# Kernel tuning notes

Hardware: AMD Instinct MI355X
Metric: run time of the kernel (lower is better)

The kernel has to match this reference:

```python
import jax, jax.numpy as jnp
import numpy as np

D_MODEL = 1024
N_HEADS = 16
D_HEAD = D_MODEL // N_HEADS


def setup_inputs() -> dict:
    key = jax.random.key(0)
    ks = jax.random.split(key, 9)
    s = 1.0 / np.sqrt(D_MODEL)
    def lin(kw, kb):
        W = jax.random.uniform(kw, (D_MODEL, D_MODEL), jnp.float32, -s, s)
        b = jax.random.uniform(kb, (D_MODEL,), jnp.float32, -s, s)
        return W, b
    Wq, bq = lin(ks[0], ks[1])
    Wk, bk = lin(ks[2], ks[3])
    Wv, bv = lin(ks[4], ks[5])
    Wo, bo = lin(ks[6], ks[7])
    x = jax.random.normal(ks[8], (4, 2048, D_MODEL), jnp.float32)
    return {"x": x, "Wq": Wq, "bq": bq, "Wk": Wk, "bk": bk,
            "Wv": Wv, "bv": bv, "Wo": Wo, "bo": bo}


def reference(x, Wq, bq, Wk, bk, Wv, bv, Wo, bo):
    B, T, C = x.shape
    # torch Linear: y = x @ W.T + b
    Q = x @ Wq.T + bq
    K = x @ Wk.T + bk
    V = x @ Wv.T + bv
    # [B, H, T, Dh]
    Q = Q.reshape(B, T, N_HEADS, D_HEAD).transpose(0, 2, 1, 3)
    K = K.reshape(B, T, N_HEADS, D_HEAD).transpose(0, 2, 1, 3)
    V = V.reshape(B, T, N_HEADS, D_HEAD).transpose(0, 2, 1, 3)
    scale = jnp.float32(np.sqrt(D_HEAD))
    scores = jnp.einsum('bhqd,bhkd->bhqk', Q, K) / scale
    causal = jnp.tril(jnp.ones((T, T), dtype=bool))  # True where allowed
    scores = jnp.where(causal, scores, jnp.float32(-jnp.inf))
    attn = jax.nn.softmax(scores, axis=-1)
    out = jnp.einsum('bhqk,bhkd->bhqd', attn, V)
    out = out.transpose(0, 2, 1, 3).reshape(B, T, C)
    return out @ Wo.T + bo
```

## Files before the change

### kernel.cpp

```cpp
#include <hip/hip_runtime.h>
#include <hip/hip_bf16.h>


typedef float f32x4 __attribute__((ext_vector_type(4)));
typedef __bf16 bf16x8 __attribute__((ext_vector_type(8)));

#define DEVI __device__ __forceinline__

#define QSCALE 0.1803368801111204f

template<int N> struct IC { static constexpr int value = N; };

DEVI ushort f2b(float x) {
  __hip_bfloat16 h = __float2bfloat16(x);
  return __builtin_bit_cast(ushort, h);
}

DEVI unsigned int pkbf(float a, float b) {
#if __has_builtin(__builtin_amdgcn_cvt_pk_bf16_f32)
  typedef __bf16 bf16x2 __attribute__((ext_vector_type(2)));
  bf16x2 r = __builtin_amdgcn_cvt_pk_bf16_f32(a, b);
  return __builtin_bit_cast(unsigned int, r);
#else
  return (unsigned int)f2b(a) | ((unsigned int)f2b(b) << 16);
#endif
}

DEVI bf16x8 ldsFrag(const ushort* p) {
  return __builtin_bit_cast(bf16x8, *(const uint4*)p);
}

DEVI f32x4 mfma16(bf16x8 a, bf16x8 b, f32x4 c) {
  return __builtin_amdgcn_mfma_f32_16x16x32_bf16(a, b, c, 0, 0, 0);
}

DEVI void gload_lds16(const ushort* g, ushort* l) {
  __builtin_amdgcn_global_load_lds(
      (const __attribute__((address_space(1))) unsigned int*)g,
      (__attribute__((address_space(3))) unsigned int*)l, 16, 0, 0);
}

#define SBAR() do { __builtin_amdgcn_sched_barrier(0); \
                    __builtin_amdgcn_s_barrier();      \
                    __builtin_amdgcn_sched_barrier(0); } while (0)

__global__ void k_cvtAll(const float4* __restrict__ x,
                         const float4* __restrict__ w0, const float4* __restrict__ w1,
                         const float4* __restrict__ w2, const float4* __restrict__ w3,
                         ushort4* __restrict__ xb, ushort4* __restrict__ wcat) {
  const int blk = blockIdx.x;
  const int i = blk * 256 + threadIdx.x;
  float4 f;
  ushort4* dst;
  int di;
  if (blk < 8192) {
    f = x[i]; dst = xb; di = i;
  } else {
    const int wi = i - 8192 * 256;
    const int sel = wi >> 18;
    const float4* src = (sel == 0) ? w0 : (sel == 1) ? w1 : (sel == 2) ? w2 : w3;
    f = src[wi & 262143]; dst = wcat; di = wi;
  }
  ushort4 o;
  o.x = f2b(f.x); o.y = f2b(f.y); o.z = f2b(f.z); o.w = f2b(f.w);
  dst[di] = o;
}

__global__ __launch_bounds__(512, 2)
void k_gemmQKV(const ushort* __restrict__ A, const ushort* __restrict__ W,
               const float* __restrict__ bq, const float* __restrict__ bk,
               const float* __restrict__ bv,
               ushort* __restrict__ oQ, ushort* __restrict__ oK,
               ushort* __restrict__ oV) {
  __shared__ ushort As[2][256 * 64];
  __shared__ ushort Bs[2][384 * 64];
  const int tid = threadIdx.x;
  const int wave = tid >> 6, lane = tid & 63;
  const int col = lane & 15, quad = lane >> 4;
  const int id = blockIdx.x;
  const int xcd = id & 7, idx = id >> 3;
  const int m0 = (xcd * 4 + (idx & 3)) * 256;
  const int nb = idx >> 2;
  const int wm = (wave >> 2) * 128;
  const int wn = (wave & 3) * 64;
  const int wnv = (wave & 3) * 32;
  const bool matQ = (nb < 4);

  const int grow = lane >> 3;
  const int gchunk = ((lane & 7) ^ grow) * 8;
  const int cswz = col & 7;
  const ushort* Ag = A + (size_t)(m0 + wave * 32 + grow) * 1024 + gchunk;

  auto bptr = [&](int u) {
    const int br = wave * 48 + u * 8;
    const int wr = (br < 256) ? (nb * 256 + br + grow)
                              : (2048 + nb * 128 + (br - 256) + grow);
    return W + (size_t)wr * 1024 + gchunk;
  };

  f32x4 aq[8][4] = {};
  f32x4 av[8][2] = {};
  bf16x8 bfr[4], bfv[2];

  auto stage6 = [&](int t1) {
    const int buf = t1 & 1;
    const int ks = t1 * 64;
#pragma unroll
    for (int u = 0; u < 4; ++u)
      gload_lds16(Ag + (size_t)u * 8 * 1024 + ks, &As[buf][(wave * 32 + u * 8) * 64]);
#pragma unroll
    for (int u = 0; u < 2; ++u)
      gload_lds16(bptr(u) + ks, &Bs[buf][(wave * 48 + u * 8) * 64]);
  };
  auto stage4 = [&](int t1) {
    const int buf = t1 & 1;
    const int ks = t1 * 64;
#pragma unroll
    for (int u = 2; u < 6; ++u)
      gload_lds16(bptr(u) + ks, &Bs[buf][(wave * 48 + u * 8) * 64]);
  };

  auto phase = [&](int p, int h, int kk, bool rdB, int dr, auto stg) {
    const int ko = ((kk * 4 + quad) ^ cswz) * 8;
    bf16x8 af[4];
#pragma unroll
    for (int i = 0; i < 4; ++i)
      af[i] = ldsFrag(&As[p][(wm + h * 64 + i * 16 + col) * 64 + ko]);
    if (rdB) {
#pragma unroll
      for (int j = 0; j < 4; ++j)
        bfr[j] = ldsFrag(&Bs[p][(wn + j * 16 + col) * 64 + ko]);
#pragma unroll
      for (int j = 0; j < 2; ++j)
        bfv[j] = ldsFrag(&Bs[p][(256 + wnv + j * 16 + col) * 64 + ko]);
    }
    stg();
    SBAR();
    asm volatile("s_waitcnt lgkmcnt(0)" ::: "memory");
    __builtin_amdgcn_sched_barrier(0);
    __builtin_amdgcn_s_setprio(1);
#pragma unroll
    for (int i = 0; i < 4; ++i)
#pragma unroll
      for (int j = 0; j < 4; ++j)
        aq[h * 4 + i][j] = mfma16(bfr[j], af[i], aq[h * 4 + i][j]);
#pragma unroll
    for (int i = 0; i < 4; ++i)
#pragma unroll
      for (int j = 0; j < 2; ++j)
        av[h * 4 + i][j] = mfma16(af[i], bfv[j], av[h * 4 + i][j]);
    __builtin_amdgcn_s_setprio(0);
    if (dr) { asm volatile("s_waitcnt vmcnt(0)" ::: "memory"); }
    SBAR();
  };

  stage6(0); stage4(0);
  asm volatile("s_waitcnt vmcnt(0)" ::: "memory");
  SBAR();

  for (int t = 0; t < 16; ++t) {
    const int p = t & 1;
    const bool st = (t < 15);
    phase(p, 0, 0, true,  0,  [&] { if (st) stage6(t + 1); });
    phase(p, 1, 0, false, 0,  [&] { if (st) stage4(t + 1); });
    phase(p, 0, 1, true,  0,  [&] {});
    phase(p, 1, 1, false, st ? 1 : 0, [&] {});
  }

  {
    ushort* dst = matQ ? oQ : oK;
    const float* bias = matQ ? bq : bk;
    const float sc = matQ ? QSCALE : 1.0f;
#pragma unroll
    for (int h = 0; h < 2; ++h)
#pragma unroll
      for (int j = 0; j < 4; ++j) {
        const int nl = (nb & 3) * 256 + wn + j * 16 + quad * 4;
        const int hh = nl >> 6, dh0 = nl & 63;
        const float4 bb = *(const float4*)&bias[nl];
#pragma unroll
        for (int i = 0; i < 4; ++i) {
          const int m = m0 + wm + h * 64 + i * 16 + col;
          const int b = m >> 11, t = m & 2047;
          ushort4 pk;
          pk.x = f2b((aq[h * 4 + i][j][0] + bb.x) * sc);
          pk.y = f2b((aq[h * 4 + i][j][1] + bb.y) * sc);
          pk.z = f2b((aq[h * 4 + i][j][2] + bb.z) * sc);
          pk.w = f2b((aq[h * 4 + i][j][3] + bb.w) * sc);
          *(ushort4*)&dst[(((size_t)(b * 16 + hh) * 2048) + t) * 64 + dh0] = pk;
        }
      }
  }
  {
#pragma unroll
    for (int h = 0; h < 2; ++h)
#pragma unroll
      for (int j = 0; j < 2; ++j) {
        const int nl = nb * 128 + wnv + j * 16 + col;
        const int hh = nl >> 6, dh = nl & 63;
        const float bn = bv[nl];
#pragma unroll
        for (int i = 0; i < 4; ++i) {
          const int mBase = m0 + wm + h * 64 + i * 16 + quad * 4;
          const int b = mBase >> 11, t = mBase & 2047;
          ushort4 pk;
          pk.x = f2b(av[h * 4 + i][j][0] + bn);
          pk.y = f2b(av[h * 4 + i][j][1] + bn);
          pk.z = f2b(av[h * 4 + i][j][2] + bn);
          pk.w = f2b(av[h * 4 + i][j][3] + bn);
          *(ushort4*)&oV[(((size_t)(b * 16 + hh) * 64) + dh) * 2048 + t] = pk;
        }
      }
  }
}

__global__ __launch_bounds__(512, 2)
void k_gemmP(const ushort* __restrict__ A, const ushort* __restrict__ W,
             const float* __restrict__ b0, float* __restrict__ outF) {
  __shared__ ushort As[3 * 128 * 64];
  __shared__ ushort Bs[3 * 256 * 64];
  const int tid = threadIdx.x;
  const int wave = tid >> 6, lane = tid & 63;
  const int col = lane & 15, quad = lane >> 4;
  const int id = blockIdx.x;
  const int s_ = id >> 3;
  const int m0 = ((id & 7) * 8 + (s_ & 7)) * 128;
  const int n0 = (s_ >> 3) * 256;
  const int wm = (wave >> 2) * 64, wn = (wave & 3) * 64;
  f32x4 acc[4][4] = {};

  const int grow = lane >> 3;
  const int gchunk = ((lane & 7) ^ grow) * 8;
  const int cswz = col & 7;
  const ushort* Ag = A + (size_t)(m0 + wave * 16 + grow) * 1024 + gchunk;
  const ushort* Wg = W + (size_t)(n0 + wave * 32 + grow) * 1024 + gchunk;
  ushort* AsW = &As[wave * 1024];
  ushort* BsW = &Bs[wave * 2048];

  auto stageA = [&](int ks, int sb) {
    gload_lds16(Ag + ks,        AsW + sb * 8192);
    gload_lds16(Ag + ks + 8192, AsW + sb * 8192 + 512);
  };
  auto stageBh = [&](int ks, int sb, int h) {
    const ushort* sp = Wg + ks + h * 16384;
    ushort* dp = BsW + sb * 16384 + h * 1024;
    gload_lds16(sp,        dp);
    gload_lds16(sp + 8192, dp + 512);
  };

  auto phase = [&](int cur, int kk, auto stagef) {
    const int ko = ((kk * 4 + quad) ^ cswz) * 8;
    const ushort* Ab = &As[cur * 8192];
    const ushort* Bb = &Bs[cur * 16384];
    bf16x8 af[4], bfr[4];
#pragma unroll
    for (int i = 0; i < 4; ++i)
      af[i] = ldsFrag(&Ab[(wm + i * 16 + col) * 64 + ko]);
#pragma unroll
    for (int j = 0; j < 4; ++j)
      bfr[j] = ldsFrag(&Bb[(wn + j * 16 + col) * 64 + ko]);
    stagef();
    SBAR();
    __builtin_amdgcn_s_setprio(1);
#pragma unroll
    for (int i = 0; i < 4; ++i)
#pragma unroll
      for (int j = 0; j < 4; ++j)
        acc[i][j] = mfma16(bfr[j], af[i], acc[i][j]);
    __builtin_amdgcn_s_setprio(0);
  };

  stageA(0, 0);  stageBh(0, 0, 0);  stageBh(0, 0, 1);
  stageA(64, 1); stageBh(64, 1, 0); stageBh(64, 1, 1);
  asm volatile("s_waitcnt vmcnt(6)" ::: "memory");
  SBAR();

  int r0 = 0, r1 = 1, r2 = 2;
  for (int t = 0; t < 14; ++t) {
    const int ks = (t + 2) * 64;
    phase(r0, 0, [&] { stageA(ks, r2); stageBh(ks, r2, 0); });
    SBAR();
    phase(r0, 1, [&] { stageBh(ks, r2, 1); });
    asm volatile("s_waitcnt vmcnt(6)" ::: "memory");
    SBAR();
    const int tmp = r0; r0 = r1; r1 = r2; r2 = tmp;
  }
  phase(r0, 0, [&] {});
  SBAR();
  phase(r0, 1, [&] {});
  asm volatile("s_waitcnt vmcnt(0)" ::: "memory");
  SBAR();
  phase(r1, 0, [&] {});
  SBAR();
  phase(r1, 1, [&] {});

#pragma unroll
  for (int j = 0; j < 4; ++j) {
    const int nb = n0 + wn + j * 16 + quad * 4;
    const float4 bb = *(const float4*)&b0[nb];
#pragma unroll
    for (int i = 0; i < 4; ++i) {
      const int m = m0 + wm + i * 16 + col;
      float4 v;
      v.x = acc[i][j][0] + bb.x;
      v.y = acc[i][j][1] + bb.y;
      v.z = acc[i][j][2] + bb.z;
      v.w = acc[i][j][3] + bb.w;
      *(float4*)&outF[(size_t)m * 1024 + nb] = v;
    }
  }
}

__global__ __launch_bounds__(512, 4)
void k_attn(const ushort* __restrict__ Q, const ushort* __restrict__ K,
            const ushort* __restrict__ Vt, ushort* __restrict__ AO) {
  __shared__ ushort Ks[2 * 4096];
  __shared__ ushort Vs[2 * 4096];
  __shared__ ushort Os[512];
  __shared__ ushort Ps[16 * 16 * 72];
  const int tid = threadIdx.x;
  const int wave = tid >> 6, lane = tid & 63;
  const int col = lane & 15, quad = lane >> 4;
  const int id = blockIdx.x;
  const int bh = (id & 7) * 8 + ((id >> 3) & 7);
  const int g = id >> 6;
  const int t = (id < 256) ? (7 - g) : (g - 4);
  const int q0 = t * 256;
  const ushort* Qg = Q + (size_t)bh * 2048 * 64;
  const ushort* Kg = K + (size_t)bh * 2048 * 64;
  const ushort* Vg = Vt + (size_t)bh * 64 * 2048;

  if (tid < 128) {
    const ushort one = 0x3F80;
    ushort4 zv;
    if (tid < 8) { zv.x = one; zv.y = one; zv.z = one; zv.w = one; }
    else         { zv.x = 0;   zv.y = 0;   zv.z = 0;   zv.w = 0;   }
    *(ushort4*)&Os[tid * 4] = zv;
  }

  const int grow = lane >> 3;
  const int gchunk = ((lane & 7) ^ grow) * 8;
  const int cswz = col & 7;
  ushort* Pw0 = &Ps[((wave * 2 + 0) * 16 + col) * 72];
  ushort* Pw1 = &Ps[((wave * 2 + 1) * 16 + col) * 72];

  bf16x8 qf[2][2];
#pragma unroll
  for (int s = 0; s < 2; ++s) {
    const ushort* p = Qg + (q0 + wave * 32 + s * 16 + col) * 64 + quad * 8;
    qf[s][0] = __builtin_bit_cast(bf16x8, *(const uint4*)p);
    qf[s][1] = __builtin_bit_cast(bf16x8, *(const uint4*)(p + 32));
  }

  f32x4 o[2][4] = {};
  f32x4 la[2] = {};

  const ushort* kPtr = Kg + (wave * 8 + grow) * 64 + gchunk;
  const ushort* vPtr = Vg + (size_t)(wave * 8 + grow) * 2048 + gchunk;

  auto stage = [&](auto bufc) {
    constexpr int BUF = decltype(bufc)::value;
    gload_lds16(kPtr, &Ks[BUF * 4096 + wave * 512]);
    gload_lds16(vPtr, &Vs[BUF * 4096 + wave * 512]);
    kPtr += 64 * 64;
    vPtr += 64;
  };

  auto step = [&](auto bufc, auto maskc, int j0) {
    constexpr int BUF = decltype(bufc)::value;
    constexpr bool MASKED = (decltype(maskc)::value != 0);
    const ushort* Kb = &Ks[BUF * 4096];
    const ushort* Vb = &Vs[BUF * 4096];
    bf16x8 kf[4][2];
#pragma unroll
    for (int i = 0; i < 4; ++i) {
      kf[i][0] = ldsFrag(&Kb[(i * 16 + col) * 64 + (((0 * 4 + quad) ^ cswz) * 8)]);
      kf[i][1] = ldsFrag(&Kb[(i * 16 + col) * 64 + (((1 * 4 + quad) ^ cswz) * 8)]);
    }
#pragma unroll
    for (int s = 0; s < 2; ++s) {
      ushort* Pw = s ? Pw1 : Pw0;
      const int dlim = MASKED ? (q0 + wave * 32 + s * 16 + col - j0 - quad * 4) : 0;
#pragma unroll
      for (int i = 0; i < 4; ++i) {
        f32x4 z = {0.f, 0.f, 0.f, 0.f};
        f32x4 sv = mfma16(kf[i][0], qf[s][0], z);
        sv = mfma16(kf[i][1], qf[s][1], sv);
        if (MASKED) {
#pragma unroll
          for (int r = 0; r < 4; ++r)
            if (i * 16 + r > dlim) sv[r] = -1e30f;
        }
        f32x4 pv;
#pragma unroll
        for (int r = 0; r < 4; ++r) pv[r] = __builtin_amdgcn_exp2f(sv[r]);
        uint2 pk;
        pk.x = pkbf(pv[0], pv[1]);
        pk.y = pkbf(pv[2], pv[3]);
        *(uint2*)&Pw[i * 16 + quad * 4] = pk;
      }
    }
    bf16x8 osf = ldsFrag(&Os[col * 32 + quad * 8]);
#pragma unroll
    for (int c = 0; c < 2; ++c) {
      bf16x8 pb0 = ldsFrag(&Pw0[c * 32 + quad * 8]);
      bf16x8 pb1 = ldsFrag(&Pw1[c * 32 + quad * 8]);
      la[0] = mfma16(osf, pb0, la[0]);
      la[1] = mfma16(osf, pb1, la[1]);
#pragma unroll
      for (int i = 0; i < 4; ++i) {
        bf16x8 vf = ldsFrag(&Vb[(i * 16 + col) * 64 + (((c * 4 + quad) ^ cswz) * 8)]);
        o[0][i] = mfma16(vf, pb0, o[0][i]);
        o[1][i] = mfma16(vf, pb1, o[1][i]);
      }
    }
  };

  __syncthreads();
  stage(IC<0>{});
  for (int it2 = 0; it2 < 2 * t; ++it2) {
    __syncthreads();
    stage(IC<1>{});
    step(IC<0>{}, IC<0>{}, 0);
    __syncthreads();
    stage(IC<0>{});
    step(IC<1>{}, IC<0>{}, 0);
  }
  __syncthreads();
  stage(IC<1>{});
  step(IC<0>{}, IC<1>{}, q0);
  __syncthreads();
  stage(IC<0>{});
  if (wave >= 2) step(IC<1>{}, IC<1>{}, q0 + 64);
  __syncthreads();
  stage(IC<1>{});
  if (wave >= 4) step(IC<0>{}, IC<1>{}, q0 + 128);
  __syncthreads();
  if (wave >= 6) step(IC<1>{}, IC<1>{}, q0 + 192);

  const float invs[2] = {1.0f / __shfl(la[0][0], col), 1.0f / __shfl(la[1][0], col)};
  const int b = bh >> 4, h = bh & 15;
#pragma unroll
  for (int s = 0; s < 2; ++s) {
    const float inv = invs[s];
    const int tq = q0 + wave * 32 + s * 16 + col;
    ushort* dst = AO + (size_t)(b * 2048 + tq) * 1024 + h * 64;
#pragma unroll
    for (int i = 0; i < 4; ++i) {
      f32x4 v = o[s][i];
      ushort4 pk;
      pk.x = f2b(v[0] * inv);
      pk.y = f2b(v[1] * inv);
      pk.z = f2b(v[2] * inv);
      pk.w = f2b(v[3] * inv);
      *(ushort4*)&dst[i * 16 + quad * 4] = pk;
    }
  }
}

extern "C" void kernel_launch(void* const* d_in, const int* in_sizes, int n_in,
                              void* d_out, int out_size, void* d_ws, size_t ws_size,
                              hipStream_t stream) {
  const float* x  = (const float*)d_in[0];
  const float* Wq = (const float*)d_in[1];
  const float* bq = (const float*)d_in[2];
  const float* Wk = (const float*)d_in[3];
  const float* bk = (const float*)d_in[4];
  const float* Wv = (const float*)d_in[5];
  const float* bv = (const float*)d_in[6];
  const float* Wo = (const float*)d_in[7];
  const float* bo = (const float*)d_in[8];
  float* out = (float*)d_out;

  char* ws = (char*)d_ws;
  ushort* xb    = (ushort*)ws;
  ushort* Wcat  = (ushort*)(ws + (size_t)16 * 1024 * 1024);
  ushort* Wob   = Wcat + (size_t)3 * 1024 * 1024;
  ushort* Qh    = (ushort*)(ws + (size_t)24 * 1024 * 1024);
  ushort* Kh    = Qh + (size_t)8192 * 1024;
  ushort* Vt    = Kh + (size_t)8192 * 1024;
  ushort* AO    = Vt + (size_t)8192 * 1024;

  k_cvtAll<<<12288, 256, 0, stream>>>((const float4*)x,
                                      (const float4*)Wq, (const float4*)Wk,
                                      (const float4*)Wv, (const float4*)Wo,
                                      (ushort4*)xb, (ushort4*)Wcat);

  k_gemmQKV<<<256, 512, 0, stream>>>(xb, Wcat, bq, bk, bv, Qh, Kh, Vt);

  k_attn<<<512, 512, 0, stream>>>(Qh, Kh, Vt, AO);

  k_gemmP<<<256, 512, 0, stream>>>(AO, Wob, bo, out);
}
```

Measured before the change: 245.9 us.

## Fuse convert, QKV GEMM, attention and projection into one cooperative persistent kernel

Replaces the four separate launches (convert, QKV GEMM, attention, output GEMM) with a single cooperative kernel of 256 blocks that runs the stages in sequence, separated by grid-wide syncs. Shared memory is one union buffer reused by each stage. Attention now handles two query tiles per block, pairing tile t with 7-t to balance the causal work. The aim is to remove launch gaps and tail effects between kernels. The cost is grid.sync overhead, lower occupancy in attention (previously 512 blocks at 4 per CU, now 256 blocks with large static LDS), and a convert stage limited to 256 blocks.

```diff
diff --git a/kernel.cpp b/kernel.cpp
--- a/kernel.cpp
+++ b/kernel.cpp
@@ -1,5 +1,8 @@
 #include <hip/hip_runtime.h>
 #include <hip/hip_bf16.h>
+#include <hip/hip_cooperative_groups.h>
+
+namespace cg = cooperative_groups;
 
 
 typedef float f32x4 __attribute__((ext_vector_type(4)));
@@ -44,416 +47,431 @@
                     __builtin_amdgcn_s_barrier();      \
                     __builtin_amdgcn_sched_barrier(0); } while (0)
 
-__global__ void k_cvtAll(const float4* __restrict__ x,
-                         const float4* __restrict__ w0, const float4* __restrict__ w1,
-                         const float4* __restrict__ w2, const float4* __restrict__ w3,
-                         ushort4* __restrict__ xb, ushort4* __restrict__ wcat) {
-  const int blk = blockIdx.x;
-  const int i = blk * 256 + threadIdx.x;
-  float4 f;
-  ushort4* dst;
-  int di;
-  if (blk < 8192) {
-    f = x[i]; dst = xb; di = i;
-  } else {
-    const int wi = i - 8192 * 256;
-    const int sel = wi >> 18;
-    const float4* src = (sel == 0) ? w0 : (sel == 1) ? w1 : (sel == 2) ? w2 : w3;
-    f = src[wi & 262143]; dst = wcat; di = wi;
-  }
-  ushort4 o;
-  o.x = f2b(f.x); o.y = f2b(f.y); o.z = f2b(f.z); o.w = f2b(f.w);
-  dst[di] = o;
-}
-
 __global__ __launch_bounds__(512, 2)
-void k_gemmQKV(const ushort* __restrict__ A, const ushort* __restrict__ W,
-               const float* __restrict__ bq, const float* __restrict__ bk,
-               const float* __restrict__ bv,
-               ushort* __restrict__ oQ, ushort* __restrict__ oK,
-               ushort* __restrict__ oV) {
-  __shared__ ushort As[2][256 * 64];
-  __shared__ ushort Bs[2][384 * 64];
+void k_fused(const float4* __restrict__ x4,
+             const float4* __restrict__ w0, const float4* __restrict__ w1,
+             const float4* __restrict__ w2, const float4* __restrict__ w3,
+             const float* __restrict__ bq, const float* __restrict__ bk,
+             const float* __restrict__ bv, const float* __restrict__ bo,
+             float* __restrict__ outF,
+             ushort* __restrict__ xb, ushort* __restrict__ Wcat,
+             ushort* __restrict__ Wob,
+             ushort* __restrict__ Qh, ushort* __restrict__ Kh,
+             ushort* __restrict__ Vt, ushort* __restrict__ AO) {
+  __shared__ __align__(16) char smem[163840];
+  cg::grid_group grid = cg::this_grid();
+
   const int tid = threadIdx.x;
   const int wave = tid >> 6, lane = tid & 63;
   const int col = lane & 15, quad = lane >> 4;
   const int id = blockIdx.x;
-  const int xcd = id & 7, idx = id >> 3;
-  const int m0 = (xcd * 4 + (idx & 3)) * 256;
-  const int nb = idx >> 2;
-  const int wm = (wave >> 2) * 128;
-  const int wn = (wave & 3) * 64;
-  const int wnv = (wave & 3) * 32;
-  const bool matQ = (nb < 4);
-
-  const int grow = lane >> 3;
-  const int gchunk = ((lane & 7) ^ grow) * 8;
-  const int cswz = col & 7;
-  const ushort* Ag = A + (size_t)(m0 + wave * 32 + grow) * 1024 + gchunk;
-
-  auto bptr = [&](int u) {
-    const int br = wave * 48 + u * 8;
-    const int wr = (br < 256) ? (nb * 256 + br + grow)
-                              : (2048 + nb * 128 + (br - 256) + grow);
-    return W + (size_t)wr * 1024 + gchunk;
-  };
-
-  f32x4 aq[8][4] = {};
-  f32x4 av[8][2] = {};
-  bf16x8 bfr[4], bfv[2];
-
-  auto stage6 = [&](int t1) {
-    const int buf = t1 & 1;
-    const int ks = t1 * 64;
-#pragma unroll
-    for (int u = 0; u < 4; ++u)
-      gload_lds16(Ag + (size_t)u * 8 * 1024 + ks, &As[buf][(wave * 32 + u * 8) * 64]);
-#pragma unroll
-    for (int u = 0; u < 2; ++u)
-      gload_lds16(bptr(u) + ks, &Bs[buf][(wave * 48 + u * 8) * 64]);
-  };
-  auto stage4 = [&](int t1) {
-    const int buf = t1 & 1;
-    const int ks = t1 * 64;
-#pragma unroll
-    for (int u = 2; u < 6; ++u)
-      gload_lds16(bptr(u) + ks, &Bs[buf][(wave * 48 + u * 8) * 64]);
-  };
-
-  auto phase = [&](int p, int h, int kk, bool rdB, int dr, auto stg) {
-    const int ko = ((kk * 4 + quad) ^ cswz) * 8;
-    bf16x8 af[4];
-#pragma unroll
-    for (int i = 0; i < 4; ++i)
-      af[i] = ldsFrag(&As[p][(wm + h * 64 + i * 16 + col) * 64 + ko]);
-    if (rdB) {
-#pragma unroll
-      for (int j = 0; j < 4; ++j)
-        bfr[j] = ldsFrag(&Bs[p][(wn + j * 16 + col) * 64 + ko]);
-#pragma unroll
-      for (int j = 0; j < 2; ++j)
-        bfv[j] = ldsFrag(&Bs[p][(256 + wnv + j * 16 + col) * 64 + ko]);
-    }
-    stg();
+
+  {
+    ushort4* xb4 = (ushort4*)xb;
+    ushort4* wc4 = (ushort4*)Wcat;
+    const int stride = 256 * 512;
+    for (int idx = id * 512 + tid; idx < 3145728; idx += stride) {
+      float4 f;
+      ushort4* dst;
+      int di;
+      if (idx < 2097152) {
+        f = x4[idx]; dst = xb4; di = idx;
+      } else {
+        const int wi = idx - 2097152;
+        const int sel = wi >> 18;
+        const float4* src = (sel == 0) ? w0 : (sel == 1) ? w1 : (sel == 2) ? w2 : w3;
+        f = src[wi & 262143]; dst = wc4; di = wi;
+      }
+      ushort4 o;
+      o.x = f2b(f.x); o.y = f2b(f.y); o.z = f2b(f.z); o.w = f2b(f.w);
+      dst[di] = o;
+    }
+  }
+
+  grid.sync();
+
+  {
+    ushort* As = (ushort*)smem;
+    ushort* Bs = (ushort*)(smem + 65536);
+    const ushort* A = xb;
+    const ushort* W = Wcat;
+    const int xcd = id & 7, idx = id >> 3;
+    const int m0 = (xcd * 4 + (idx & 3)) * 256;
+    const int nb = idx >> 2;
+    const int wm = (wave >> 2) * 128;
+    const int wn = (wave & 3) * 64;
+    const int wnv = (wave & 3) * 32;
+    const bool matQ = (nb < 4);
+
+    const int grow = lane >> 3;
+    const int gchunk = ((lane & 7) ^ grow) * 8;
+    const int cswz = col & 7;
+    const ushort* Ag = A + (size_t)(m0 + wave * 32 + grow) * 1024 + gchunk;
+
+    auto bptr = [&](int u) {
+      const int br = wave * 48 + u * 8;
+      const int wr = (br < 256) ? (nb * 256 + br + grow)
+                                : (2048 + nb * 128 + (br - 256) + grow);
+      return W + (size_t)wr * 1024 + gchunk;
+    };
+
+    f32x4 aq[8][4] = {};
+    f32x4 av[8][2] = {};
+    bf16x8 bfr[4], bfv[2];
+
+    auto stage6 = [&](int t1) {
+      const int buf = t1 & 1;
+      const int ks = t1 * 64;
+#pragma unroll
+      for (int u = 0; u < 4; ++u)
+        gload_lds16(Ag + (size_t)u * 8 * 1024 + ks,
+                    &As[buf * 16384 + (wave * 32 + u * 8) * 64]);
+#pragma unroll
+      for (int u = 0; u < 2; ++u)
+        gload_lds16(bptr(u) + ks, &Bs[buf * 24576 + (wave * 48 + u * 8) * 64]);
+    };
+    auto stage4 = [&](int t1) {
+      const int buf = t1 & 1;
+      const int ks = t1 * 64;
+#pragma unroll
+      for (int u = 2; u < 6; ++u)
+        gload_lds16(bptr(u) + ks, &Bs[buf * 24576 + (wave * 48 + u * 8) * 64]);
+    };
+
+    auto phase = [&](int p, int h, int kk, bool rdB, int dr, auto stg) {
+      const int ko = ((kk * 4 + quad) ^ cswz) * 8;
+      bf16x8 af[4];
+#pragma unroll
+      for (int i = 0; i < 4; ++i)
+        af[i] = ldsFrag(&As[p * 16384 + (wm + h * 64 + i * 16 + col) * 64 + ko]);
+      if (rdB) {
+#pragma unroll
+        for (int j = 0; j < 4; ++j)
+          bfr[j] = ldsFrag(&Bs[p * 24576 + (wn + j * 16 + col) * 64 + ko]);
+#pragma unroll
+        for (int j = 0; j < 2; ++j)
+          bfv[j] = ldsFrag(&Bs[p * 24576 + (256 + wnv + j * 16 + col) * 64 + ko]);
+      }
+      stg();
+      SBAR();
+      asm volatile("s_waitcnt lgkmcnt(0)" ::: "memory");
+      __builtin_amdgcn_sched_barrier(0);
+      __builtin_amdgcn_s_setprio(1);
+#pragma unroll
+      for (int i = 0; i < 4; ++i)
+#pragma unroll
+        for (int j = 0; j < 4; ++j)
+          aq[h * 4 + i][j] = mfma16(bfr[j], af[i], aq[h * 4 + i][j]);
+#pragma unroll
+      for (int i = 0; i < 4; ++i)
+#pragma unroll
+        for (int j = 0; j < 2; ++j)
+          av[h * 4 + i][j] = mfma16(af[i], bfv[j], av[h * 4 + i][j]);
+      __builtin_amdgcn_s_setprio(0);
+      if (dr) { asm volatile("s_waitcnt vmcnt(0)" ::: "memory"); }
+      SBAR();
+    };
+
+    stage6(0); stage4(0);
+    asm volatile("s_waitcnt vmcnt(0)" ::: "memory");
     SBAR();
-    asm volatile("s_waitcnt lgkmcnt(0)" ::: "memory");
-    __builtin_amdgcn_sched_barrier(0);
-    __builtin_amdgcn_s_setprio(1);
-#pragma unroll
-    for (int i = 0; i < 4; ++i)
-#pragma unroll
-      for (int j = 0; j < 4; ++j)
-        aq[h * 4 + i][j] = mfma16(bfr[j], af[i], aq[h * 4 + i][j]);
-#pragma unroll
-    for (int i = 0; i < 4; ++i)
-#pragma unroll
-      for (int j = 0; j < 2; ++j)
-        av[h * 4 + i][j] = mfma16(af[i], bfv[j], av[h * 4 + i][j]);
-    __builtin_amdgcn_s_setprio(0);
-    if (dr) { asm volatile("s_waitcnt vmcnt(0)" ::: "memory"); }
-    SBAR();
-  };
-
-  stage6(0); stage4(0);
-  asm volatile("s_waitcnt vmcnt(0)" ::: "memory");
-  SBAR();
-
-  for (int t = 0; t < 16; ++t) {
-    const int p = t & 1;
-    const bool st = (t < 15);
-    phase(p, 0, 0, true,  0,  [&] { if (st) stage6(t + 1); });
-    phase(p, 1, 0, false, 0,  [&] { if (st) stage4(t + 1); });
-    phase(p, 0, 1, true,  0,  [&] {});
-    phase(p, 1, 1, false, st ? 1 : 0, [&] {});
+
+    for (int t = 0; t < 16; ++t) {
+      const int p = t & 1;
+      const bool st = (t < 15);
+      phase(p, 0, 0, true,  0,  [&] { if (st) stage6(t + 1); });
+      phase(p, 1, 0, false, 0,  [&] { if (st) stage4(t + 1); });
+      phase(p, 0, 1, true,  0,  [&] {});
+      phase(p, 1, 1, false, st ? 1 : 0, [&] {});
+    }
+
+    {
+      ushort* dst = matQ ? Qh : Kh;
+      const float* bias = matQ ? bq : bk;
+      const float sc = matQ ? QSCALE : 1.0f;
+#pragma unroll
+      for (int h = 0; h < 2; ++h)
+#pragma unroll
+        for (int j = 0; j < 4; ++j) {
+          const int nl = (nb & 3) * 256 + wn + j * 16 + quad * 4;
+          const int hh = nl >> 6, dh0 = nl & 63;
+          const float4 bb = *(const float4*)&bias[nl];
+#pragma unroll
+          for (int i = 0; i < 4; ++i) {
+            const int m = m0 + wm + h * 64 + i * 16 + col;
+            const int b = m >> 11, t = m & 2047;
+            ushort4 pk;
+            pk.x = f2b((aq[h * 4 + i][j][0] + bb.x) * sc);
+            pk.y = f2b((aq[h * 4 + i][j][1] + bb.y) * sc);
+            pk.z = f2b((aq[h * 4 + i][j][2] + bb.z) * sc);
+            pk.w = f2b((aq[h * 4 + i][j][3] + bb.w) * sc);
+            *(ushort4*)&dst[(((size_t)(b * 16 + hh) * 2048) + t) * 64 + dh0] = pk;
+          }
+        }
+    }
+    {
+#pragma unroll
+      for (int h = 0; h < 2; ++h)
+#pragma unroll
+        for (int j = 0; j < 2; ++j) {
+          const int nl = nb * 128 + wnv + j * 16 + col;
+          const int hh = nl >> 6, dh = nl & 63;
+          const float bn = bv[nl];
+#pragma unroll
+          for (int i = 0; i < 4; ++i) {
+            const int mBase = m0 + wm + h * 64 + i * 16 + quad * 4;
+            const int b = mBase >> 11, t = mBase & 2047;
+            ushort4 pk;
+            pk.x = f2b(av[h * 4 + i][j][0] + bn);
+            pk.y = f2b(av[h * 4 + i][j][1] + bn);
+            pk.z = f2b(av[h * 4 + i][j][2] + bn);
+            pk.w = f2b(av[h * 4 + i][j][3] + bn);
+            *(ushort4*)&Vt[(((size_t)(b * 16 + hh) * 64) + dh) * 2048 + t] = pk;
+          }
+        }
+    }
   }
 
+  grid.sync();
+
   {
-    ushort* dst = matQ ? oQ : oK;
-    const float* bias = matQ ? bq : bk;
-    const float sc = matQ ? QSCALE : 1.0f;
-#pragma unroll
-    for (int h = 0; h < 2; ++h)
-#pragma unroll
-      for (int j = 0; j < 4; ++j) {
-        const int nl = (nb & 3) * 256 + wn + j * 16 + quad * 4;
-        const int hh = nl >> 6, dh0 = nl & 63;
-        const float4 bb = *(const float4*)&bias[nl];
+    ushort* Ks = (ushort*)smem;
+    ushort* Vs = Ks + 8192;
+    ushort* Os = Vs + 8192;
+    ushort* Ps = Os + 512;
+    const int bh = (id & 7) * 8 + ((id >> 3) & 7);
+    const int pr = id >> 6;
+    const ushort* Qg = Qh + (size_t)bh * 2048 * 64;
+    const ushort* Kg = Kh + (size_t)bh * 2048 * 64;
+    const ushort* Vg = Vt + (size_t)bh * 64 * 2048;
+
+    __syncthreads();
+    if (tid < 128) {
+      const ushort one = 0x3F80;
+      ushort4 zv;
+      if (tid < 8) { zv.x = one; zv.y = one; zv.z = one; zv.w = one; }
+      else         { zv.x = 0;   zv.y = 0;   zv.z = 0;   zv.w = 0;   }
+      *(ushort4*)&Os[tid * 4] = zv;
+    }
+
+    const int grow = lane >> 3;
+    const int gchunk = ((lane & 7) ^ grow) * 8;
+    const int cswz = col & 7;
+    ushort* Pw0 = &Ps[((wave * 2 + 0) * 16 + col) * 72];
+    ushort* Pw1 = &Ps[((wave * 2 + 1) * 16 + col) * 72];
+
+    for (int pp = 0; pp < 2; ++pp) {
+      const int t = pp ? (7 - pr) : pr;
+      const int q0 = t * 256;
+
+      bf16x8 qf[2][2];
+#pragma unroll
+      for (int s = 0; s < 2; ++s) {
+        const ushort* p = Qg + (q0 + wave * 32 + s * 16 + col) * 64 + quad * 8;
+        qf[s][0] = __builtin_bit_cast(bf16x8, *(const uint4*)p);
+        qf[s][1] = __builtin_bit_cast(bf16x8, *(const uint4*)(p + 32));
+      }
+
+      f32x4 o[2][4] = {};
+      f32x4 la[2] = {};
+
+      const ushort* kPtr = Kg + (wave * 8 + grow) * 64 + gchunk;
+      const ushort* vPtr = Vg + (size_t)(wave * 8 + grow) * 2048 + gchunk;
+
+      auto stage = [&](auto bufc) {
+        constexpr int BUF = decltype(bufc)::value;
+        gload_lds16(kPtr, &Ks[BUF * 4096 + wave * 512]);
+        gload_lds16(vPtr, &Vs[BUF * 4096 + wave * 512]);
+        kPtr += 64 * 64;
+        vPtr += 64;
+      };
+
+      auto step = [&](auto bufc, auto maskc, int j0) {
+        constexpr int BUF = decltype(bufc)::value;
+        constexpr bool MASKED = (decltype(maskc)::value != 0);
+        const ushort* Kb = &Ks[BUF * 4096];
+        const ushort* Vb = &Vs[BUF * 4096];
+        bf16x8 kf[4][2];
 #pragma unroll
         for (int i = 0; i < 4; ++i) {
-          const int m = m0 + wm + h * 64 + i * 16 + col;
-          const int b = m >> 11, t = m & 2047;
+          kf[i][0] = ldsFrag(&Kb[(i * 16 + col) * 64 + (((0 * 4 + quad) ^ cswz) * 8)]);
+          kf[i][1] = ldsFrag(&Kb[(i * 16 + col) * 64 + (((1 * 4 + quad) ^ cswz) * 8)]);
+        }
+#pragma unroll
+        for (int s = 0; s < 2; ++s) {
+          ushort* Pw = s ? Pw1 : Pw0;
+          const int dlim = MASKED ? (q0 + wave * 32 + s * 16 + col - j0 - quad * 4) : 0;
+#pragma unroll
+          for (int i = 0; i < 4; ++i) {
+            f32x4 z = {0.f, 0.f, 0.f, 0.f};
+            f32x4 sv = mfma16(kf[i][0], qf[s][0], z);
+            sv = mfma16(kf[i][1], qf[s][1], sv);
+            if (MASKED) {
+#pragma unroll
+              for (int r = 0; r < 4; ++r)
+                if (i * 16 + r > dlim) sv[r] = -1e30f;
+            }
+            f32x4 pv;
+#pragma unroll
+            for (int r = 0; r < 4; ++r) pv[r] = __builtin_amdgcn_exp2f(sv[r]);
+            uint2 pk;
+            pk.x = pkbf(pv[0], pv[1]);
+            pk.y = pkbf(pv[2], pv[3]);
+            *(uint2*)&Pw[i * 16 + quad * 4] = pk;
+          }
+        }
+        bf16x8 osf = ldsFrag(&Os[col * 32 + quad * 8]);
+#pragma unroll
+        for (int c = 0; c < 2; ++c) {
+          bf16x8 pb0 = ldsFrag(&Pw0[c * 32 + quad * 8]);
+          bf16x8 pb1 = ldsFrag(&Pw1[c * 32 + quad * 8]);
+          la[0] = mfma16(osf, pb0, la[0]);
+          la[1] = mfma16(osf, pb1, la[1]);
+#pragma unroll
+          for (int i = 0; i < 4; ++i) {
+            bf16x8 vf = ldsFrag(&Vb[(i * 16 + col) * 64 + (((c * 4 + quad) ^ cswz) * 8)]);
+            o[0][i] = mfma16(vf, pb0, o[0][i]);
+            o[1][i] = mfma16(vf, pb1, o[1][i]);
+          }
+        }
+      };
+
+      __syncthreads();
+      stage(IC<0>{});
+      for (int it2 = 0; it2 < 2 * t; ++it2) {
+        __syncthreads();
+        stage(IC<1>{});
+        step(IC<0>{}, IC<0>{}, 0);
+        __syncthreads();
+        stage(IC<0>{});
+        step(IC<1>{}, IC<0>{}, 0);
+      }
+      __syncthreads();
+      stage(IC<1>{});
+      step(IC<0>{}, IC<1>{}, q0);
+      __syncthreads();
+      stage(IC<0>{});
+      if (wave >= 2) step(IC<1>{}, IC<1>{}, q0 + 64);
+      __syncthreads();
+      stage(IC<1>{});
+      if (wave >= 4) step(IC<0>{}, IC<1>{}, q0 + 128);
+      __syncthreads();
+      if (wave >= 6) step(IC<1>{}, IC<1>{}, q0 + 192);
+
+      const float invs[2] = {1.0f / __shfl(la[0][0], col), 1.0f / __shfl(la[1][0], col)};
+      const int b = bh >> 4, h = bh & 15;
+#pragma unroll
+      for (int s = 0; s < 2; ++s) {
+        const float inv = invs[s];
+        const int tq = q0 + wave * 32 + s * 16 + col;
+        ushort* dst = AO + (size_t)(b * 2048 + tq) * 1024 + h * 64;
+#pragma unroll
+        for (int i = 0; i < 4; ++i) {
+          f32x4 v = o[s][i];
           ushort4 pk;
-          pk.x = f2b((aq[h * 4 + i][j][0] + bb.x) * sc);
-          pk.y = f2b((aq[h * 4 + i][j][1] + bb.y) * sc);
-          pk.z = f2b((aq[h * 4 + i][j][2] + bb.z) * sc);
-          pk.w = f2b((aq[h * 4 + i][j][3] + bb.w) * sc);
-          *(ushort4*)&dst[(((size_t)(b * 16 + hh) * 2048) + t) * 64 + dh0] = pk;
+          pk.x = f2b(v[0] * inv);
+          pk.y = f2b(v[1] * inv);
+          pk.z = f2b(v[2] * inv);
+          pk.w = f2b(v[3] * inv);
+          *(ushort4*)&dst[i * 16 + quad * 4] = pk;
         }
       }
+    }
   }
+
+  grid.sync();
+
   {
-#pragma unroll
-    for (int h = 0; h < 2; ++h)
-#pragma unroll
-      for (int j = 0; j < 2; ++j) {
-        const int nl = nb * 128 + wnv + j * 16 + col;
-        const int hh = nl >> 6, dh = nl & 63;
-        const float bn = bv[nl];
-#pragma unroll
-        for (int i = 0; i < 4; ++i) {
-          const int mBase = m0 + wm + h * 64 + i * 16 + quad * 4;
-          const int b = mBase >> 11, t = mBase & 2047;
-          ushort4 pk;
-          pk.x = f2b(av[h * 4 + i][j][0] + bn);
-          pk.y = f2b(av[h * 4 + i][j][1] + bn);
-          pk.z = f2b(av[h * 4 + i][j][2] + bn);
-          pk.w = f2b(av[h * 4 + i][j][3] + bn);
-          *(ushort4*)&oV[(((size_t)(b * 16 + hh) * 64) + dh) * 2048 + t] = pk;
-        }
-      }
-  }
-}
-
-__global__ __launch_bounds__(512, 2)
-void k_gemmP(const ushort* __restrict__ A, const ushort* __restrict__ W,
-             const float* __restrict__ b0, float* __restrict__ outF) {
-  __shared__ ushort As[3 * 128 * 64];
-  __shared__ ushort Bs[3 * 256 * 64];
-  const int tid = threadIdx.x;
-  const int wave = tid >> 6, lane = tid & 63;
-  const int col = lane & 15, quad = lane >> 4;
-  const int id = blockIdx.x;
-  const int s_ = id >> 3;
-  const int m0 = ((id & 7) * 8 + (s_ & 7)) * 128;
-  const int n0 = (s_ >> 3) * 256;
-  const int wm = (wave >> 2) * 64, wn = (wave & 3) * 64;
-  f32x4 acc[4][4] = {};
-
-  const int grow = lane >> 3;
-  const int gchunk = ((lane & 7) ^ grow) * 8;
-  const int cswz = col & 7;
-  const ushort* Ag = A + (size_t)(m0 + wave * 16 + grow) * 1024 + gchunk;
-  const ushort* Wg = W + (size_t)(n0 + wave * 32 + grow) * 1024 + gchunk;
-  ushort* AsW = &As[wave * 1024];
-  ushort* BsW = &Bs[wave * 2048];
-
-  auto stageA = [&](int ks, int sb) {
-    gload_lds16(Ag + ks,        AsW + sb * 8192);
-    gload_lds16(Ag + ks + 8192, AsW + sb * 8192 + 512);
-  };
-  auto stageBh = [&](int ks, int sb, int h) {
-    const ushort* sp = Wg + ks + h * 16384;
-    ushort* dp = BsW + sb * 16384 + h * 1024;
-    gload_lds16(sp,        dp);
-    gload_lds16(sp + 8192, dp + 512);
-  };
-
-  auto phase = [&](int cur, int kk, auto stagef) {
-    const int ko = ((kk * 4 + quad) ^ cswz) * 8;
-    const ushort* Ab = &As[cur * 8192];
-    const ushort* Bb = &Bs[cur * 16384];
-    bf16x8 af[4], bfr[4];
-#pragma unroll
-    for (int i = 0; i < 4; ++i)
-      af[i] = ldsFrag(&Ab[(wm + i * 16 + col) * 64 + ko]);
-#pragma unroll
-    for (int j = 0; j < 4; ++j)
-      bfr[j] = ldsFrag(&Bb[(wn + j * 16 + col) * 64 + ko]);
-    stagef();
-    SBAR();
-    __builtin_amdgcn_s_setprio(1);
-#pragma unroll
-    for (int i = 0; i < 4; ++i)
+    ushort* As = (ushort*)smem;
+    ushort* Bs = (ushort*)(smem + 49152);
+    const ushort* A = AO;
+    const ushort* W = Wob;
+    const int s_ = id >> 3;
+    const int m0 = ((id & 7) * 8 + (s_ & 7)) * 128;
+    const int n0 = (s_ >> 3) * 256;
+    const int wm = (wave >> 2) * 64, wn = (wave & 3) * 64;
+    f32x4 acc[4][4] = {};
+
+    const int grow = lane >> 3;
+    const int gchunk = ((lane & 7) ^ grow) * 8;
+    const int cswz = col & 7;
+    const ushort* Ag = A + (size_t)(m0 + wave * 16 + grow) * 1024 + gchunk;
+    const ushort* Wg = W + (size_t)(n0 + wave * 32 + grow) * 1024 + gchunk;
+    ushort* AsW = &As[wave * 1024];
+    ushort* BsW = &Bs[wave * 2048];
+
+    auto stageA = [&](int ks, int sb) {
+      gload_lds16(Ag + ks,        AsW + sb * 8192);
+      gload_lds16(Ag + ks + 8192, AsW + sb * 8192 + 512);
+    };
+    auto stageBh = [&](int ks, int sb, int h) {
+      const ushort* sp = Wg + ks + h * 16384;
+      ushort* dp = BsW + sb * 16384 + h * 1024;
+      gload_lds16(sp,        dp);
+      gload_lds16(sp + 8192, dp + 512);
+    };
+
+    auto phase = [&](int cur, int kk, auto stagef) {
+      const int ko = ((kk * 4 + quad) ^ cswz) * 8;
+      const ushort* Ab = &As[cur * 8192];
+      const ushort* Bb = &Bs[cur * 16384];
+      bf16x8 af[4], bfr[4];
+#pragma unroll
+      for (int i = 0; i < 4; ++i)
+        af[i] = ldsFrag(&Ab[(wm + i * 16 + col) * 64 + ko]);
 #pragma unroll
       for (int j = 0; j < 4; ++j)
-        acc[i][j] = mfma16(bfr[j], af[i], acc[i][j]);
-    __builtin_amdgcn_s_setprio(0);
-  };
-
-  stageA(0, 0);  stageBh(0, 0, 0);  stageBh(0, 0, 1);
-  stageA(64, 1); stageBh(64, 1, 0); stageBh(64, 1, 1);
-  asm volatile("s_waitcnt vmcnt(6)" ::: "memory");
-  SBAR();
-
-  int r0 = 0, r1 = 1, r2 = 2;
-  for (int t = 0; t < 14; ++t) {
-    const int ks = (t + 2) * 64;
-    phase(r0, 0, [&] { stageA(ks, r2); stageBh(ks, r2, 0); });
-    SBAR();
-    phase(r0, 1, [&] { stageBh(ks, r2, 1); });
+        bfr[j] = ldsFrag(&Bb[(wn + j * 16 + col) * 64 + ko]);
+      stagef();
+      SBAR();
+      __builtin_amdgcn_s_setprio(1);
+#pragma unroll
+      for (int i = 0; i < 4; ++i)
+#pragma unroll
+        for (int j = 0; j < 4; ++j)
+          acc[i][j] = mfma16(bfr[j], af[i], acc[i][j]);
+      __builtin_amdgcn_s_setprio(0);
+    };
+
+    __syncthreads();
+    stageA(0, 0);  stageBh(0, 0, 0);  stageBh(0, 0, 1);
+    stageA(64, 1); stageBh(64, 1, 0); stageBh(64, 1, 1);
     asm volatile("s_waitcnt vmcnt(6)" ::: "memory");
     SBAR();
-    const int tmp = r0; r0 = r1; r1 = r2; r2 = tmp;
-  }
-  phase(r0, 0, [&] {});
-  SBAR();
-  phase(r0, 1, [&] {});
-  asm volatile("s_waitcnt vmcnt(0)" ::: "memory");
-  SBAR();
-  phase(r1, 0, [&] {});
-  SBAR();
-  phase(r1, 1, [&] {});
-
-#pragma unroll
-  for (int j = 0; j < 4; ++j) {
-    const int nb = n0 + wn + j * 16 + quad * 4;
-    const float4 bb = *(const float4*)&b0[nb];
-#pragma unroll
-    for (int i = 0; i < 4; ++i) {
-      const int m = m0 + wm + i * 16 + col;
-      float4 v;
-      v.x = acc[i][j][0] + bb.x;
-      v.y = acc[i][j][1] + bb.y;
-      v.z = acc[i][j][2] + bb.z;
-      v.w = acc[i][j][3] + bb.w;
-      *(float4*)&outF[(size_t)m * 1024 + nb] = v;
-    }
-  }
-}
-
-__global__ __launch_bounds__(512, 4)
-void k_attn(const ushort* __restrict__ Q, const ushort* __restrict__ K,
-            const ushort* __restrict__ Vt, ushort* __restrict__ AO) {
-  __shared__ ushort Ks[2 * 4096];
-  __shared__ ushort Vs[2 * 4096];
-  __shared__ ushort Os[512];
-  __shared__ ushort Ps[16 * 16 * 72];
-  const int tid = threadIdx.x;
-  const int wave = tid >> 6, lane = tid & 63;
-  const int col = lane & 15, quad = lane >> 4;
-  const int id = blockIdx.x;
-  const int bh = (id & 7) * 8 + ((id >> 3) & 7);
-  const int g = id >> 6;
-  const int t = (id < 256) ? (7 - g) : (g - 4);
-  const int q0 = t * 256;
-  const ushort* Qg = Q + (size_t)bh * 2048 * 64;
-  const ushort* Kg = K + (size_t)bh * 2048 * 64;
-  const ushort* Vg = Vt + (size_t)bh * 64 * 2048;
-
-  if (tid < 128) {
-    const ushort one = 0x3F80;
-    ushort4 zv;
-    if (tid < 8) { zv.x = one; zv.y = one; zv.z = one; zv.w = one; }
-    else         { zv.x = 0;   zv.y = 0;   zv.z = 0;   zv.w = 0;   }
-    *(ushort4*)&Os[tid * 4] = zv;
-  }
-
-  const int grow = lane >> 3;
-  const int gchunk = ((lane & 7) ^ grow) * 8;
-  const int cswz = col & 7;
-  ushort* Pw0 = &Ps[((wave * 2 + 0) * 16 + col) * 72];
-  ushort* Pw1 = &Ps[((wave * 2 + 1) * 16 + col) * 72];
-
-  bf16x8 qf[2][2];
-#pragma unroll
-  for (int s = 0; s < 2; ++s) {
-    const ushort* p = Qg + (q0 + wave * 32 + s * 16 + col) * 64 + quad * 8;
-    qf[s][0] = __builtin_bit_cast(bf16x8, *(const uint4*)p);
-    qf[s][1] = __builtin_bit_cast(bf16x8, *(const uint4*)(p + 32));
-  }
-
-  f32x4 o[2][4] = {};
-  f32x4 la[2] = {};
-
-  const ushort* kPtr = Kg + (wave * 8 + grow) * 64 + gchunk;
-  const ushort* vPtr = Vg + (size_t)(wave * 8 + grow) * 2048 + gchunk;
-
-  auto stage = [&](auto bufc) {
-    constexpr int BUF = decltype(bufc)::value;
-    gload_lds16(kPtr, &Ks[BUF * 4096 + wave * 512]);
-    gload_lds16(vPtr, &Vs[BUF * 4096 + wave * 512]);
-    kPtr += 64 * 64;
-    vPtr += 64;
-  };
-
-  auto step = [&](auto bufc, auto maskc, int j0) {
-    constexpr int BUF = decltype(bufc)::value;
-    constexpr bool MASKED = (decltype(maskc)::value != 0);
-    const ushort* Kb = &Ks[BUF * 4096];
-    const ushort* Vb = &Vs[BUF * 4096];
-    bf16x8 kf[4][2];
-#pragma unroll
-    for (int i = 0; i < 4; ++i) {
-      kf[i][0] = ldsFrag(&Kb[(i * 16 + col) * 64 + (((0 * 4 + quad) ^ cswz) * 8)]);
-      kf[i][1] = ldsFrag(&Kb[(i * 16 + col) * 64 + (((1 * 4 + quad) ^ cswz) * 8)]);
-    }
-#pragma unroll
-    for (int s = 0; s < 2; ++s) {
-      ushort* Pw = s ? Pw1 : Pw0;
-      const int dlim = MASKED ? (q0 + wave * 32 + s * 16 + col - j0 - quad * 4) : 0;
+
+    int r0 = 0, r1 = 1, r2 = 2;
+    for (int t = 0; t < 14; ++t) {
+      const int ks = (t + 2) * 64;
+      phase(r0, 0, [&] { stageA(ks, r2); stageBh(ks, r2, 0); });
+      SBAR();
+      phase(r0, 1, [&] { stageBh(ks, r2, 1); });
+      asm volatile("s_waitcnt vmcnt(6)" ::: "memory");
+      SBAR();
+      const int tmp = r0; r0 = r1; r1 = r2; r2 = tmp;
+    }
+    phase(r0, 0, [&] {});
+    SBAR();
+    phase(r0, 1, [&] {});
+    asm volatile("s_waitcnt vmcnt(0)" ::: "memory");
+    SBAR();
+    phase(r1, 0, [&] {});
+    SBAR();
+    phase(r1, 1, [&] {});
+
+#pragma unroll
+    for (int j = 0; j < 4; ++j) {
+      const int nb = n0 + wn + j * 16 + quad * 4;
+      const float4 bb = *(const float4*)&bo[nb];
 #pragma unroll
       for (int i = 0; i < 4; ++i) {
-        f32x4 z = {0.f, 0.f, 0.f, 0.f};
-        f32x4 sv = mfma16(kf[i][0], qf[s][0], z);
-        sv = mfma16(kf[i][1], qf[s][1], sv);
-        if (MASKED) {
-#pragma unroll
-          for (int r = 0; r < 4; ++r)
-            if (i * 16 + r > dlim) sv[r] = -1e30f;
-        }
-        f32x4 pv;
-#pragma unroll
-        for (int r = 0; r < 4; ++r) pv[r] = __builtin_amdgcn_exp2f(sv[r]);
-        uint2 pk;
-        pk.x = pkbf(pv[0], pv[1]);
-        pk.y = pkbf(pv[2], pv[3]);
-        *(uint2*)&Pw[i * 16 + quad * 4] = pk;
+        const int m = m0 + wm + i * 16 + col;
+        float4 v;
+        v.x = acc[i][j][0] + bb.x;
+        v.y = acc[i][j][1] + bb.y;
+        v.z = acc[i][j][2] + bb.z;
+        v.w = acc[i][j][3] + bb.w;
+        *(float4*)&outF[(size_t)m * 1024 + nb] = v;
       }
-    }
-    bf16x8 osf = ldsFrag(&Os[col * 32 + quad * 8]);
-#pragma unroll
-    for (int c = 0; c < 2; ++c) {
-      bf16x8 pb0 = ldsFrag(&Pw0[c * 32 + quad * 8]);
-      bf16x8 pb1 = ldsFrag(&Pw1[c * 32 + quad * 8]);
-      la[0] = mfma16(osf, pb0, la[0]);
-      la[1] = mfma16(osf, pb1, la[1]);
-#pragma unroll
-      for (int i = 0; i < 4; ++i) {
-        bf16x8 vf = ldsFrag(&Vb[(i * 16 + col) * 64 + (((c * 4 + quad) ^ cswz) * 8)]);
-        o[0][i] = mfma16(vf, pb0, o[0][i]);
-        o[1][i] = mfma16(vf, pb1, o[1][i]);
-      }
-    }
-  };
-
-  __syncthreads();
-  stage(IC<0>{});
-  for (int it2 = 0; it2 < 2 * t; ++it2) {
-    __syncthreads();
-    stage(IC<1>{});
-    step(IC<0>{}, IC<0>{}, 0);
-    __syncthreads();
-    stage(IC<0>{});
-    step(IC<1>{}, IC<0>{}, 0);
-  }
-  __syncthreads();
-  stage(IC<1>{});
-  step(IC<0>{}, IC<1>{}, q0);
-  __syncthreads();
-  stage(IC<0>{});
-  if (wave >= 2) step(IC<1>{}, IC<1>{}, q0 + 64);
-  __syncthreads();
-  stage(IC<1>{});
-  if (wave >= 4) step(IC<0>{}, IC<1>{}, q0 + 128);
-  __syncthreads();
-  if (wave >= 6) step(IC<1>{}, IC<1>{}, q0 + 192);
-
-  const float invs[2] = {1.0f / __shfl(la[0][0], col), 1.0f / __shfl(la[1][0], col)};
-  const int b = bh >> 4, h = bh & 15;
-#pragma unroll
-  for (int s = 0; s < 2; ++s) {
-    const float inv = invs[s];
-    const int tq = q0 + wave * 32 + s * 16 + col;
-    ushort* dst = AO + (size_t)(b * 2048 + tq) * 1024 + h * 64;
-#pragma unroll
-    for (int i = 0; i < 4; ++i) {
-      f32x4 v = o[s][i];
-      ushort4 pk;
-      pk.x = f2b(v[0] * inv);
-      pk.y = f2b(v[1] * inv);
-      pk.z = f2b(v[2] * inv);
-      pk.w = f2b(v[3] * inv);
-      *(ushort4*)&dst[i * 16 + quad * 4] = pk;
     }
   }
 }
@@ -461,15 +479,15 @@
 extern "C" void kernel_launch(void* const* d_in, const int* in_sizes, int n_in,
                               void* d_out, int out_size, void* d_ws, size_t ws_size,
                               hipStream_t stream) {
-  const float* x  = (const float*)d_in[0];
-  const float* Wq = (const float*)d_in[1];
-  const float* bq = (const float*)d_in[2];
-  const float* Wk = (const float*)d_in[3];
-  const float* bk = (const float*)d_in[4];
-  const float* Wv = (const float*)d_in[5];
-  const float* bv = (const float*)d_in[6];
-  const float* Wo = (const float*)d_in[7];
-  const float* bo = (const float*)d_in[8];
+  const float4* x4 = (const float4*)d_in[0];
+  const float4* Wq = (const float4*)d_in[1];
+  const float*  bq = (const float*)d_in[2];
+  const float4* Wk = (const float4*)d_in[3];
+  const float*  bk = (const float*)d_in[4];
+  const float4* Wv = (const float4*)d_in[5];
+  const float*  bv = (const float*)d_in[6];
+  const float4* Wo = (const float4*)d_in[7];
+  const float*  bo = (const float*)d_in[8];
   float* out = (float*)d_out;
 
   char* ws = (char*)d_ws;
@@ -481,14 +499,13 @@
   ushort* Vt    = Kh + (size_t)8192 * 1024;
   ushort* AO    = Vt + (size_t)8192 * 1024;
 
-  k_cvtAll<<<12288, 256, 0, stream>>>((const float4*)x,
-                                      (const float4*)Wq, (const float4*)Wk,
-                                      (const float4*)Wv, (const float4*)Wo,
-                                      (ushort4*)xb, (ushort4*)Wcat);
-
-  k_gemmQKV<<<256, 512, 0, stream>>>(xb, Wcat, bq, bk, bv, Qh, Kh, Vt);
-
-  k_attn<<<512, 512, 0, stream>>>(Qh, Kh, Vt, AO);
-
-  k_gemmP<<<256, 512, 0, stream>>>(AO, Wob, bo, out);
-}
+  void* args[] = {
+    (void*)&x4, (void*)&Wq, (void*)&Wk, (void*)&Wv, (void*)&Wo,
+    (void*)&bq, (void*)&bk, (void*)&bv, (void*)&bo,
+    (void*)&out,
+    (void*)&xb, (void*)&Wcat, (void*)&Wob,
+    (void*)&Qh, (void*)&Kh, (void*)&Vt, (void*)&AO
+  };
+  hipLaunchCooperativeKernel((const void*)k_fused, dim3(256), dim3(512),
+                             args, 0, stream);
+}
```

New measurement: 398.3 us. +62.0%, slower.
